# Kernel tuning notes

Hardware: AMD Instinct MI355X
Metric: run time of the kernel (lower is better)

The kernel has to match this reference:

```python
import jax, jax.numpy as jnp
import numpy as np

B, S, E, H = 4, 1024, 1024, 16
D = E // H  # head_dim = 64


def setup_inputs() -> dict:
    key = jax.random.key(0)
    ks = jax.random.split(key, 12)
    s = 1.0 / np.sqrt(E)
    return {
        "query": jax.random.normal(ks[0], (B, S, E), jnp.float32),
        "key_": jax.random.normal(ks[1], (B, S, E), jnp.float32),
        "value": jax.random.normal(ks[2], (B, S, E), jnp.float32),
        "mask": jnp.ones((B, S, S), dtype=bool),
        "Wq": jax.random.uniform(ks[3], (E, E), jnp.float32, -s, s),
        "bq": jax.random.uniform(ks[4], (E,), jnp.float32, -s, s),
        "Wk": jax.random.uniform(ks[5], (E, E), jnp.float32, -s, s),
        "bk": jax.random.uniform(ks[6], (E,), jnp.float32, -s, s),
        "Wv": jax.random.uniform(ks[7], (E, E), jnp.float32, -s, s),
        "bv": jax.random.uniform(ks[8], (E,), jnp.float32, -s, s),
        "Wo": jax.random.uniform(ks[9], (E, E), jnp.float32, -s, s),
        "bo": jax.random.uniform(ks[10], (E,), jnp.float32, -s, s),
    }


def reference(query, key_, value, mask, Wq, bq, Wk, bk, Wv, bv, Wo, bo):
    # project and split heads: [B,S,E] -> [B,H,S,D]
    def heads(x, W, b):
        return (x @ W + b).reshape(B, -1, H, D).transpose(0, 2, 1, 3)

    q = heads(query, Wq, bq)
    k = heads(key_, Wk, bk)
    v = heads(value, Wv, bv)

    scores = jnp.einsum("bhqd,bhkd->bhqk", q, k) / jnp.sqrt(jnp.float32(D))
    # bool mask: positions where mask==0 are filled with -1e9
    scores = jnp.where(mask[:, None, :, :], scores, jnp.float32(-1e9))
    attn_weights = jax.nn.softmax(scores, axis=-1)  # [B,H,Sq,Sk]
    out = jnp.einsum("bhqk,bhkd->bhqd", attn_weights, v)
    out = out.transpose(0, 2, 1, 3).reshape(B, -1, E)  # [B,Sq,E]
    attn_output = out @ Wo + bo
    return attn_output, attn_weights
```

## Files before the change

### kernel.cpp

```cpp
#include <hip/hip_runtime.h>
#include <stdint.h>

typedef __bf16 bf16;
typedef bf16 bf16x2 __attribute__((ext_vector_type(2)));
typedef bf16 bf16x4 __attribute__((ext_vector_type(4)));
typedef bf16 bf16x8 __attribute__((ext_vector_type(8)));
typedef float f32x4 __attribute__((ext_vector_type(4)));
typedef float f32x16 __attribute__((ext_vector_type(16)));

static constexpr int Bc = 4, Sc = 1024, Ec = 1024, Hc = 16, Dc = 64, BSc = 4096;

__device__ __forceinline__ void gld_lds16(const void* g, void* s) {
  __builtin_amdgcn_global_load_lds((const __attribute__((address_space(1))) void*)g,
                                   (__attribute__((address_space(3))) void*)s, 16, 0, 0);
}

__global__ void detect_mask_kernel(const uint8_t* __restrict__ mask, int* flag) {
  if (threadIdx.x == 0 && blockIdx.x == 0) {
    bool everyGroupHasZero = true;
    bool anyNonzero = false;
    for (int j = 0; j < 16; ++j) {
      bool z = false;
      for (int bjj = 0; bjj < 4; ++bjj) {
        uint8_t byte = mask[4 * j + bjj];
        if (byte == 0) z = true;
        if (byte != 0) anyNonzero = true;
      }
      if (!z) everyGroupHasZero = false;
    }
    flag[0] = (everyGroupHasZero && anyNonzero) ? 4 : 1;
    flag[1] = 1;
  }
}

__global__ __launch_bounds__(256) void scan_mask_kernel(const uint8_t* __restrict__ mask,
                                                        int* __restrict__ mflag) {
  const int stride = mflag[0];
  bool ok = true;
  const uint4* p = (const uint4*)mask;
  if (stride == 1) {
    const int n = (Bc * Sc * Sc) / 16;
    for (int i = blockIdx.x * blockDim.x + threadIdx.x; i < n; i += gridDim.x * blockDim.x) {
      uint4 w = p[i];
      uint32_t z = 0;
      z |= (w.x - 0x01010101u) & ~w.x;
      z |= (w.y - 0x01010101u) & ~w.y;
      z |= (w.z - 0x01010101u) & ~w.z;
      z |= (w.w - 0x01010101u) & ~w.w;
      if (z & 0x80808080u) ok = false;
    }
  } else {
    const int n = (Bc * Sc * Sc) / 4;
    for (int i = blockIdx.x * blockDim.x + threadIdx.x; i < n; i += gridDim.x * blockDim.x) {
      uint4 w = p[i];
      if (w.x == 0u || w.y == 0u || w.z == 0u || w.w == 0u) ok = false;
    }
  }
  if (!ok) atomicAnd(&mflag[1], 0);
}

__global__ __launch_bounds__(256) void convert_x_kernel(
    const float* __restrict__ q, const float* __restrict__ k, const float* __restrict__ v,
    bf16* __restrict__ xb) {
  const int n4 = (BSc * Ec) / 4;
  for (int i = blockIdx.x * blockDim.x + threadIdx.x; i < 3 * n4; i += gridDim.x * blockDim.x) {
    int which = i / n4;
    int off = i - which * n4;
    const float4* src = (which == 0) ? (const float4*)q : (which == 1) ? (const float4*)k : (const float4*)v;
    float4 f = src[off];
    bf16x4 o;
    o[0] = (bf16)f.x; o[1] = (bf16)f.y; o[2] = (bf16)f.z; o[3] = (bf16)f.w;
    *(bf16x4*)(xb + (size_t)which * BSc * Ec + (size_t)off * 4) = o;
  }
}

__global__ __launch_bounds__(256) void convtrans_w_kernel(
    const float* __restrict__ Wq, const float* __restrict__ Wk,
    const float* __restrict__ Wv, const float* __restrict__ Wo,
    bf16* __restrict__ wT) {
  __shared__ float tile[64][65];
  const int k0 = blockIdx.x * 64, n0 = blockIdx.y * 64, z = blockIdx.z;
  const float* W = (z == 0) ? Wq : (z == 1) ? Wk : (z == 2) ? Wv : Wo;
  bf16* out = wT + (size_t)z * Ec * Ec;
  const int t = threadIdx.x;
#pragma unroll
  for (int p = 0; p < 16; p++) {
    int r = p * 4 + (t >> 6), c = t & 63;
    tile[r][c] = W[(size_t)(k0 + r) * Ec + n0 + c];
  }
  __syncthreads();
#pragma unroll
  for (int p = 0; p < 8; p++) {
    int n = p * 8 + (t >> 5), kk = (t & 31) * 2;
    bf16x2 v2;
    v2[0] = (bf16)tile[kk][n];
    v2[1] = (bf16)tile[kk + 1][n];
    *(bf16x2*)(out + (size_t)(n0 + n) * Ec + k0 + kk) = v2;
  }
}

template <int MODE>
__global__ __launch_bounds__(256) void gemm128_kernel(
    const bf16* __restrict__ A_, const bf16* __restrict__ W_,
    const float* __restrict__ bias0, const float* __restrict__ bias1, const float* __restrict__ bias2,
    bf16* __restrict__ outb_, float* __restrict__ outf) {
  constexpr int K = 1024, N = 1024;
  const int z = blockIdx.z;
  const bf16* A = A_ + (size_t)z * BSc * K;
  const bf16* Wt = W_ + (size_t)z * N * K;
  const float* bias = (z == 0) ? bias0 : (z == 1) ? bias1 : bias2;
  bf16* outb = outb_ + (size_t)z * Bc * Hc * Sc * Dc;
  const float oscale = (MODE == 1 && z == 0) ? 0.125f : 1.0f;
  const int n0 = blockIdx.x * 128, m0 = blockIdx.y * 128;

  __shared__ bf16 As[128 * 64];
  __shared__ bf16 Bs[128 * 64];
  const int t = threadIdx.x, wave = t >> 6, lane = t & 63;
  const int wr = wave >> 1, wc = wave & 1;

  f32x4 acc[4][4];
#pragma unroll
  for (int i = 0; i < 4; i++)
#pragma unroll
    for (int j = 0; j < 4; j++)
#pragma unroll
      for (int r = 0; r < 4; r++) acc[i][j][r] = 0.f;

  const int srow = (lane >> 3);
  const int scol = (lane & 7) * 8;

  for (int kt = 0; kt < K; kt += 64) {
#pragma unroll
    for (int i = 0; i < 4; i++) {
      const int chunk = i * 4 + wave;
      const int row = chunk * 8 + srow;
      gld_lds16(A + (size_t)(m0 + row) * K + kt + scol, &As[chunk * 512]);
      gld_lds16(Wt + (size_t)(n0 + row) * K + kt + scol, &Bs[chunk * 512]);
    }
    __syncthreads();
#pragma unroll
    for (int kk = 0; kk < 2; kk++) {
      bf16x8 af[4], bg[4];
#pragma unroll
      for (int i = 0; i < 4; i++) {
        af[i] = *(const bf16x8*)&As[(64 * wr + i * 16 + (lane & 15)) * 64 + kk * 32 + (lane >> 4) * 8];
        bg[i] = *(const bf16x8*)&Bs[(64 * wc + i * 16 + (lane & 15)) * 64 + kk * 32 + (lane >> 4) * 8];
      }
#pragma unroll
      for (int mi = 0; mi < 4; mi++)
#pragma unroll
        for (int ni = 0; ni < 4; ni++)
          acc[mi][ni] = __builtin_amdgcn_mfma_f32_16x16x32_bf16(af[mi], bg[ni], acc[mi][ni], 0, 0, 0);
    }
    __syncthreads();
  }

#pragma unroll
  for (int mi = 0; mi < 4; mi++) {
#pragma unroll
    for (int ni = 0; ni < 4; ni++) {
      const int col = n0 + 64 * wc + ni * 16 + (lane & 15);
      const float bvl = bias[col];
#pragma unroll
      for (int r = 0; r < 4; r++) {
        const int row = m0 + 64 * wr + mi * 16 + (lane >> 4) * 4 + r;
        const float v = (acc[mi][ni][r] + bvl) * oscale;
        if (MODE == 0) {
          outf[(size_t)row * N + col] = v;
        } else {
          const int bidx = row >> 10, s = row & 1023, hh = col >> 6, d = col & 63;
          const int dst = (z == 1) ? (d ^ ((s & 7) << 3)) : d;
          outb[(((size_t)bidx * Hc + hh) * Sc + s) * Dc + dst] = (bf16)v;
        }
      }
    }
  }
}

__global__ __launch_bounds__(256) void transpose_v_kernel(const bf16* __restrict__ Vb,
                                                          bf16* __restrict__ VTb) {
  __shared__ bf16 tile[64][66];
  const int s0 = blockIdx.x * 64, bh = blockIdx.y;
  const bf16* src = Vb + (size_t)bh * Sc * Dc;
  bf16* dst = VTb + (size_t)bh * Dc * Sc;
  const int t = threadIdx.x;
#pragma unroll
  for (int p = 0; p < 8; p++) {
    int s = p * 8 + (t >> 5), d = (t & 31) * 2;
    *(bf16x2*)&tile[s][d] = *(const bf16x2*)(src + (size_t)(s0 + s) * Dc + d);
  }
  __syncthreads();
#pragma unroll
  for (int p = 0; p < 8; p++) {
    int d = p * 8 + (t >> 5), s = (t & 31) * 2;
    bf16x2 v2;
    v2[0] = tile[s][d];
    v2[1] = tile[s + 1][d];
    const int sidx = (s0 + s) ^ ((d & 7) << 3);
    *(bf16x2*)(dst + (size_t)d * Sc + sidx) = v2;
  }
}

__device__ __forceinline__ f32x16 qk_lds(const char* sK, const bf16x8 qf[4],
                                         int koff, int l31, int hi) {
  const int row = koff + l31;
  const char* base = sK + row * 128;
  const int sw = (row & 7) << 4;
  f32x16 a;
#pragma unroll
  for (int r = 0; r < 16; r++) a[r] = 0.f;
#pragma unroll
  for (int ks = 0; ks < 4; ks++) {
    const bf16x8 kf = *(const bf16x8*)(base + ((ks * 32 + hi * 16) ^ sw));
    a = __builtin_amdgcn_mfma_f32_32x32x16_bf16(kf, qf[ks], a, 0, 0, 0);
  }
  return a;
}

__device__ __forceinline__ void mask_app(f32x16& a, int kt, const uint8_t* mrow1,
                                         const uint8_t* mrow4, int mstride, int hi) {
  if (mstride == 1) {
#pragma unroll
    for (int gg = 0; gg < 4; gg++) {
      const int kg = kt + gg * 8 + hi * 4;
      const uint32_t mw = *(const uint32_t*)(mrow1 + kg);
#pragma unroll
      for (int r = 0; r < 4; r++)
        if (((mw >> (8 * r)) & 0xffu) == 0u) a[gg * 4 + r] = -1e9f;
    }
  } else {
#pragma unroll
    for (int gg = 0; gg < 4; gg++) {
      const int kg = kt + gg * 8 + hi * 4;
      const uint4 m4 = *(const uint4*)(mrow4 + (size_t)4 * kg);
      const uint32_t w[4] = {m4.x, m4.y, m4.z, m4.w};
#pragma unroll
      for (int r = 0; r < 4; r++)
        if (w[r] == 0u) a[gg * 4 + r] = -1e9f;
    }
  }
}

__global__ __launch_bounds__(256, 2) void attn_kernel(
    const bf16* __restrict__ Qb, const bf16* __restrict__ Kb, const bf16* __restrict__ VTb,
    const uint8_t* __restrict__ mask, const int* __restrict__ mflag,
    float* __restrict__ wout_, bf16* __restrict__ ctx) {
  const int qg = blockIdx.x, h = blockIdx.y, b = blockIdx.z;
  const int bh = b * Hc + h;
  const int t = threadIdx.x, wave = t >> 6, lane = t & 63;
  const int l31 = lane & 31, hi = lane >> 5;
  const int q0 = qg * 128 + wave * 32;
  const int q = q0 + l31;

  __shared__ __attribute__((aligned(16))) char smem[75776];
  bf16* Ptb = (bf16*)(smem + 65536) + wave * 1280;

  const bf16* Qp = Qb + ((size_t)bh * Sc + q) * Dc;
  bf16x8 qf[4];
#pragma unroll
  for (int ks = 0; ks < 4; ks++) qf[ks] = *(const bf16x8*)(Qp + ks * 16 + hi * 8);

  const int allTrue = mflag[1];
  const int mstride = mflag[0];
  const uint8_t* mrow1 = mask + (size_t)(b * Sc + q) * Sc;
  const uint8_t* mrow4 = mask + (size_t)(b * Sc + q) * Sc * 4;

  const char* Kbb = (const char*)(Kb + (size_t)bh * Sc * Dc);
  const char* VTbb = (const char*)(VTb + (size_t)bh * Dc * Sc);

  float m = -3.0e38f, l = 0.f;
#pragma unroll
  for (int j = 0; j < 4; j++) {
    const int off = j * 4096 + wave * 1024;
    gld_lds16(Kbb + off + lane * 16, smem + off);
  }
  __syncthreads();
  for (int st8 = 0; st8 < 8; st8++) {
    const int cur = st8 & 1;
    if (st8 < 7) {
#pragma unroll
      for (int j = 0; j < 4; j++) {
        const int off = j * 4096 + wave * 1024;
        gld_lds16(Kbb + (st8 + 1) * 16384 + off + lane * 16,
                  smem + (cur ^ 1) * 16384 + off);
      }
    }
    const char* sK = smem + cur * 16384;
#pragma unroll
    for (int tl = 0; tl < 4; tl++) {
      f32x16 a = qk_lds(sK, qf, tl * 32, l31, hi);
      if (!allTrue) mask_app(a, st8 * 128 + tl * 32, mrow1, mrow4, mstride, hi);
      float tm = a[0];
#pragma unroll
      for (int r = 1; r < 16; r++) tm = fmaxf(tm, a[r]);
      const float mnew = fmaxf(m, tm);
      float s = 0.f;
#pragma unroll
      for (int r = 0; r < 16; r++) s += __expf(a[r] - mnew);
      l = l * __expf(m - mnew) + s;
      m = mnew;
    }
    __syncthreads();
  }
  {
    const float mo = __shfl_xor(m, 32), lo = __shfl_xor(l, 32);
    const float M = fmaxf(m, mo);
    l = l * __expf(m - M) + lo * __expf(mo - M);
    m = M;
  }
  const float invl = 1.f / l;

  float* wbase = wout_ + ((size_t)bh * Sc + q0) * Sc;
  f32x16 oacc[2];
#pragma unroll
  for (int nj = 0; nj < 2; nj++)
#pragma unroll
    for (int r = 0; r < 16; r++) oacc[nj][r] = 0.f;

#pragma unroll
  for (int j = 0; j < 4; j++) {
    const int off = j * 4096 + wave * 1024;
    gld_lds16(Kbb + off + lane * 16, smem + off);
    const int goff = off + lane * 16;
    const int d = goff >> 8, ko = goff & 255;
    gld_lds16(VTbb + (size_t)d * 2048 + ko, smem + 32768 + off);
  }
  __syncthreads();
  for (int st8 = 0; st8 < 8; st8++) {
    const int cur = st8 & 1;
    if (st8 < 7) {
#pragma unroll
      for (int j = 0; j < 4; j++) {
        const int off = j * 4096 + wave * 1024;
        gld_lds16(Kbb + (st8 + 1) * 16384 + off + lane * 16,
                  smem + (cur ^ 1) * 16384 + off);
        const int goff = off + lane * 16;
        const int d = goff >> 8, ko = goff & 255;
        gld_lds16(VTbb + (size_t)d * 2048 + (st8 + 1) * 256 + ko,
                  smem + 32768 + (cur ^ 1) * 16384 + off);
      }
    }
    const char* sK = smem + cur * 16384;
    const char* sV = smem + 32768 + cur * 16384;
#pragma unroll
    for (int tl = 0; tl < 4; tl++) {
      f32x16 a = qk_lds(sK, qf, tl * 32, l31, hi);
      if (!allTrue) mask_app(a, st8 * 128 + tl * 32, mrow1, mrow4, mstride, hi);
#pragma unroll
      for (int gg = 0; gg < 4; gg++) {
        bf16x4 p4;
#pragma unroll
        for (int r = 0; r < 4; r++) p4[r] = (bf16)(__expf(a[gg * 4 + r] - m) * invl);
        *(bf16x4*)&Ptb[l31 * 40 + gg * 8 + hi * 4] = p4;
      }
#pragma unroll
      for (int i = 0; i < 4; i++) {
        const int q2 = 8 * i + (lane >> 3), kk = (lane & 7) * 4;
        const bf16x4 pv4 = *(const bf16x4*)&Ptb[q2 * 40 + kk];
        f32x4 v4;
#pragma unroll
        for (int r = 0; r < 4; r++) v4[r] = (float)pv4[r];
        __builtin_nontemporal_store(v4,
            (f32x4*)(wbase + (size_t)q2 * Sc + st8 * 128 + tl * 32 + kk));
      }
#pragma unroll
      for (int st = 0; st < 2; st++) {
        const bf16x8 pa = *(const bf16x8*)&Ptb[l31 * 40 + st * 16 + hi * 8];
#pragma unroll
        for (int nj = 0; nj < 2; nj++) {
          const int d = nj * 32 + l31;
          const int off = ((tl * 32 + st * 16 + hi * 8) * 2) ^ ((d & 7) << 4);
          const bf16x8 bv = *(const bf16x8*)(sV + d * 256 + off);
          oacc[nj] = __builtin_amdgcn_mfma_f32_32x32x16_bf16(pa, bv, oacc[nj], 0, 0, 0);
        }
      }
    }
    __syncthreads();
  }

#pragma unroll
  for (int nj = 0; nj < 2; nj++) {
#pragma unroll
    for (int rg = 0; rg < 16; rg++) {
      const int qq = (rg & 3) + 8 * (rg >> 2) + 4 * hi;
      Ptb[qq * 40 + l31] = (bf16)oacc[nj][rg];
    }
    const int rr = lane >> 1, c0 = (lane & 1) * 16;
    const bf16x8 o0 = *(const bf16x8*)&Ptb[rr * 40 + c0];
    const bf16x8 o1 = *(const bf16x8*)&Ptb[rr * 40 + c0 + 8];
    bf16* cbase = ctx + ((size_t)(b * Sc + q0 + rr)) * Ec + h * Dc + nj * 32 + c0;
    *(bf16x8*)cbase = o0;
    *(bf16x8*)(cbase + 8) = o1;
  }
}

extern "C" void kernel_launch(void* const* d_in, const int* in_sizes, int n_in,
                              void* d_out, int out_size, void* d_ws, size_t ws_size,
                              hipStream_t stream) {
  const float* q = (const float*)d_in[0];
  const float* k = (const float*)d_in[1];
  const float* v = (const float*)d_in[2];
  const uint8_t* mask = (const uint8_t*)d_in[3];
  const float* Wq = (const float*)d_in[4];
  const float* bq = (const float*)d_in[5];
  const float* Wk = (const float*)d_in[6];
  const float* bk = (const float*)d_in[7];
  const float* Wv = (const float*)d_in[8];
  const float* bv = (const float*)d_in[9];
  const float* Wo = (const float*)d_in[10];
  const float* bo = (const float*)d_in[11];

  bf16* wsb = (bf16*)d_ws;
  bf16* xb = wsb;
  bf16* ctx = wsb;
  bf16* VTb = wsb + (size_t)4 * 1024 * 1024;
  bf16* wT = wsb + (size_t)12 * 1024 * 1024;
  bf16* Qb = wsb + (size_t)16 * 1024 * 1024;
  bf16* Kb = wsb + (size_t)20 * 1024 * 1024;
  bf16* Vb = wsb + (size_t)24 * 1024 * 1024;
  int* mflag = (int*)((char*)d_ws + (size_t)56 * 1024 * 1024);

  float* outf = (float*)d_out;
  float* attnw = outf + (size_t)4 * 1024 * 1024;

  detect_mask_kernel<<<1, 64, 0, stream>>>(mask, mflag);
  scan_mask_kernel<<<1024, 256, 0, stream>>>(mask, mflag);
  convert_x_kernel<<<2048, 256, 0, stream>>>(q, k, v, xb);
  convtrans_w_kernel<<<dim3(16, 16, 4), 256, 0, stream>>>(Wq, Wk, Wv, Wo, wT);
  gemm128_kernel<1><<<dim3(8, 32, 3), 256, 0, stream>>>(xb, wT, bq, bk, bv, Qb, nullptr);
  transpose_v_kernel<<<dim3(16, 64), 256, 0, stream>>>(Vb, VTb);
  attn_kernel<<<dim3(8, 16, 4), 256, 0, stream>>>(Qb, Kb, VTb, mask, mflag, attnw, ctx);
  gemm128_kernel<0><<<dim3(8, 32, 1), 256, 0, stream>>>(ctx, wT + (size_t)3 * 1024 * 1024,
                                                        bo, bo, bo, nullptr, outf);
}
```

Before: 192.4 us.

## Merge prep kernels into one launch and halve attention K/V tiles for occupancy

Folds the mask scan, the activation conversion and the weight transpose-convert into one prep kernel, cutting two launches and letting these independent jobs overlap. The scan blocks now recompute the mask stride themselves instead of reading it from the flag buffer. The attention kernel streams K/V in 64-key tiles rather than 128, roughly halving LDS use so three blocks fit per CU instead of two. The cost is twice as many barrier/prefetch iterations in attention and more register pressure under the tighter launch bound.

```diff
diff --git a/kernel.cpp b/kernel.cpp
--- a/kernel.cpp
+++ b/kernel.cpp
@@ -33,69 +33,79 @@
   }
 }
 
-__global__ __launch_bounds__(256) void scan_mask_kernel(const uint8_t* __restrict__ mask,
-                                                        int* __restrict__ mflag) {
-  const int stride = mflag[0];
-  bool ok = true;
-  const uint4* p = (const uint4*)mask;
-  if (stride == 1) {
-    const int n = (Bc * Sc * Sc) / 16;
-    for (int i = blockIdx.x * blockDim.x + threadIdx.x; i < n; i += gridDim.x * blockDim.x) {
-      uint4 w = p[i];
-      uint32_t z = 0;
-      z |= (w.x - 0x01010101u) & ~w.x;
-      z |= (w.y - 0x01010101u) & ~w.y;
-      z |= (w.z - 0x01010101u) & ~w.z;
-      z |= (w.w - 0x01010101u) & ~w.w;
-      if (z & 0x80808080u) ok = false;
-    }
+__global__ __launch_bounds__(256) void prep_kernel(
+    const float* __restrict__ q, const float* __restrict__ k, const float* __restrict__ v,
+    bf16* __restrict__ xb, const uint8_t* __restrict__ mask, int* __restrict__ mflag,
+    const float* __restrict__ Wq, const float* __restrict__ Wk,
+    const float* __restrict__ Wv, const float* __restrict__ Wo, bf16* __restrict__ wT) {
+  __shared__ float tile[64][65];
+  const int bid = blockIdx.x, t = threadIdx.x;
+
+  if (bid < 2048) {
+    const int n4 = (BSc * Ec) / 4;
+    for (int i = bid * 256 + t; i < 3 * n4; i += 2048 * 256) {
+      int which = i / n4;
+      int off = i - which * n4;
+      const float4* src = (which == 0) ? (const float4*)q : (which == 1) ? (const float4*)k : (const float4*)v;
+      float4 f = src[off];
+      bf16x4 o;
+      o[0] = (bf16)f.x; o[1] = (bf16)f.y; o[2] = (bf16)f.z; o[3] = (bf16)f.w;
+      *(bf16x4*)(xb + (size_t)which * BSc * Ec + (size_t)off * 4) = o;
+    }
+  } else if (bid < 3072) {
+    bool everyGroupHasZero = true, anyNonzero = false;
+    for (int j = 0; j < 16; ++j) {
+      bool z = false;
+      for (int bjj = 0; bjj < 4; ++bjj) {
+        uint8_t byte = mask[4 * j + bjj];
+        if (byte == 0) z = true;
+        if (byte != 0) anyNonzero = true;
+      }
+      if (!z) everyGroupHasZero = false;
+    }
+    const int stride = (everyGroupHasZero && anyNonzero) ? 4 : 1;
+    bool ok = true;
+    const uint4* p = (const uint4*)mask;
+    const int sb = bid - 2048;
+    if (stride == 1) {
+      const int n = (Bc * Sc * Sc) / 16;
+      for (int i = sb * 256 + t; i < n; i += 1024 * 256) {
+        uint4 w = p[i];
+        uint32_t z = 0;
+        z |= (w.x - 0x01010101u) & ~w.x;
+        z |= (w.y - 0x01010101u) & ~w.y;
+        z |= (w.z - 0x01010101u) & ~w.z;
+        z |= (w.w - 0x01010101u) & ~w.w;
+        if (z & 0x80808080u) ok = false;
+      }
+    } else {
+      const int n = (Bc * Sc * Sc) / 4;
+      for (int i = sb * 256 + t; i < n; i += 1024 * 256) {
+        uint4 w = p[i];
+        if (w.x == 0u || w.y == 0u || w.z == 0u || w.w == 0u) ok = false;
+      }
+    }
+    if (!ok) atomicAnd(&mflag[1], 0);
   } else {
-    const int n = (Bc * Sc * Sc) / 4;
-    for (int i = blockIdx.x * blockDim.x + threadIdx.x; i < n; i += gridDim.x * blockDim.x) {
-      uint4 w = p[i];
-      if (w.x == 0u || w.y == 0u || w.z == 0u || w.w == 0u) ok = false;
-    }
-  }
-  if (!ok) atomicAnd(&mflag[1], 0);
-}
-
-__global__ __launch_bounds__(256) void convert_x_kernel(
-    const float* __restrict__ q, const float* __restrict__ k, const float* __restrict__ v,
-    bf16* __restrict__ xb) {
-  const int n4 = (BSc * Ec) / 4;
-  for (int i = blockIdx.x * blockDim.x + threadIdx.x; i < 3 * n4; i += gridDim.x * blockDim.x) {
-    int which = i / n4;
-    int off = i - which * n4;
-    const float4* src = (which == 0) ? (const float4*)q : (which == 1) ? (const float4*)k : (const float4*)v;
-    float4 f = src[off];
-    bf16x4 o;
-    o[0] = (bf16)f.x; o[1] = (bf16)f.y; o[2] = (bf16)f.z; o[3] = (bf16)f.w;
-    *(bf16x4*)(xb + (size_t)which * BSc * Ec + (size_t)off * 4) = o;
-  }
-}
-
-__global__ __launch_bounds__(256) void convtrans_w_kernel(
-    const float* __restrict__ Wq, const float* __restrict__ Wk,
-    const float* __restrict__ Wv, const float* __restrict__ Wo,
-    bf16* __restrict__ wT) {
-  __shared__ float tile[64][65];
-  const int k0 = blockIdx.x * 64, n0 = blockIdx.y * 64, z = blockIdx.z;
-  const float* W = (z == 0) ? Wq : (z == 1) ? Wk : (z == 2) ? Wv : Wo;
-  bf16* out = wT + (size_t)z * Ec * Ec;
-  const int t = threadIdx.x;
-#pragma unroll
-  for (int p = 0; p < 16; p++) {
-    int r = p * 4 + (t >> 6), c = t & 63;
-    tile[r][c] = W[(size_t)(k0 + r) * Ec + n0 + c];
-  }
-  __syncthreads();
-#pragma unroll
-  for (int p = 0; p < 8; p++) {
-    int n = p * 8 + (t >> 5), kk = (t & 31) * 2;
-    bf16x2 v2;
-    v2[0] = (bf16)tile[kk][n];
-    v2[1] = (bf16)tile[kk + 1][n];
-    *(bf16x2*)(out + (size_t)(n0 + n) * Ec + k0 + kk) = v2;
+    const int i = bid - 3072;
+    const int z = i >> 8, rem = i & 255;
+    const int k0 = (rem & 15) * 64, n0 = (rem >> 4) * 64;
+    const float* W = (z == 0) ? Wq : (z == 1) ? Wk : (z == 2) ? Wv : Wo;
+    bf16* out = wT + (size_t)z * Ec * Ec;
+#pragma unroll
+    for (int p2 = 0; p2 < 16; p2++) {
+      int r = p2 * 4 + (t >> 6), c = t & 63;
+      tile[r][c] = W[(size_t)(k0 + r) * Ec + n0 + c];
+    }
+    __syncthreads();
+#pragma unroll
+    for (int p2 = 0; p2 < 8; p2++) {
+      int n = p2 * 8 + (t >> 5), kk = (t & 31) * 2;
+      bf16x2 v2;
+      v2[0] = (bf16)tile[kk][n];
+      v2[1] = (bf16)tile[kk + 1][n];
+      *(bf16x2*)(out + (size_t)(n0 + n) * Ec + k0 + kk) = v2;
+    }
   }
 }
 
@@ -241,7 +251,7 @@
   }
 }
 
-__global__ __launch_bounds__(256, 2) void attn_kernel(
+__global__ __launch_bounds__(256, 3) void attn_kernel(
     const bf16* __restrict__ Qb, const bf16* __restrict__ Kb, const bf16* __restrict__ VTb,
     const uint8_t* __restrict__ mask, const int* __restrict__ mflag,
     float* __restrict__ wout_, bf16* __restrict__ ctx) {
@@ -252,8 +262,8 @@
   const int q0 = qg * 128 + wave * 32;
   const int q = q0 + l31;
 
-  __shared__ __attribute__((aligned(16))) char smem[75776];
-  bf16* Ptb = (bf16*)(smem + 65536) + wave * 1280;
+  __shared__ __attribute__((aligned(16))) char smem[43008];
+  bf16* Ptb = (bf16*)(smem + 32768) + wave * 1280;
 
   const bf16* Qp = Qb + ((size_t)bh * Sc + q) * Dc;
   bf16x8 qf[4];
@@ -270,26 +280,25 @@
 
   float m = -3.0e38f, l = 0.f;
 #pragma unroll
-  for (int j = 0; j < 4; j++) {
+  for (int j = 0; j < 2; j++) {
     const int off = j * 4096 + wave * 1024;
     gld_lds16(Kbb + off + lane * 16, smem + off);
   }
   __syncthreads();
-  for (int st8 = 0; st8 < 8; st8++) {
-    const int cur = st8 & 1;
-    if (st8 < 7) {
-#pragma unroll
-      for (int j = 0; j < 4; j++) {
+  for (int st = 0; st < 16; st++) {
+    const int cur = st & 1;
+    if (st < 15) {
+#pragma unroll
+      for (int j = 0; j < 2; j++) {
         const int off = j * 4096 + wave * 1024;
-        gld_lds16(Kbb + (st8 + 1) * 16384 + off + lane * 16,
-                  smem + (cur ^ 1) * 16384 + off);
-      }
-    }
-    const char* sK = smem + cur * 16384;
-#pragma unroll
-    for (int tl = 0; tl < 4; tl++) {
+        gld_lds16(Kbb + (st + 1) * 8192 + off + lane * 16, smem + (cur ^ 1) * 8192 + off);
+      }
+    }
+    const char* sK = smem + cur * 8192;
+#pragma unroll
+    for (int tl = 0; tl < 2; tl++) {
       f32x16 a = qk_lds(sK, qf, tl * 32, l31, hi);
-      if (!allTrue) mask_app(a, st8 * 128 + tl * 32, mrow1, mrow4, mstride, hi);
+      if (!allTrue) mask_app(a, st * 64 + tl * 32, mrow1, mrow4, mstride, hi);
       float tm = a[0];
 #pragma unroll
       for (int r = 1; r < 16; r++) tm = fmaxf(tm, a[r]);
@@ -318,34 +327,33 @@
     for (int r = 0; r < 16; r++) oacc[nj][r] = 0.f;
 
 #pragma unroll
-  for (int j = 0; j < 4; j++) {
+  for (int j = 0; j < 2; j++) {
     const int off = j * 4096 + wave * 1024;
     gld_lds16(Kbb + off + lane * 16, smem + off);
     const int goff = off + lane * 16;
-    const int d = goff >> 8, ko = goff & 255;
-    gld_lds16(VTbb + (size_t)d * 2048 + ko, smem + 32768 + off);
+    const int d = goff >> 7, ko = goff & 127;
+    gld_lds16(VTbb + (size_t)d * 2048 + ko, smem + 16384 + off);
   }
   __syncthreads();
-  for (int st8 = 0; st8 < 8; st8++) {
-    const int cur = st8 & 1;
-    if (st8 < 7) {
-#pragma unroll
-      for (int j = 0; j < 4; j++) {
+  for (int st = 0; st < 16; st++) {
+    const int cur = st & 1;
+    if (st < 15) {
+#pragma unroll
+      for (int j = 0; j < 2; j++) {
         const int off = j * 4096 + wave * 1024;
-        gld_lds16(Kbb + (st8 + 1) * 16384 + off + lane * 16,
-                  smem + (cur ^ 1) * 16384 + off);
+        gld_lds16(Kbb + (st + 1) * 8192 + off + lane * 16, smem + (cur ^ 1) * 8192 + off);
         const int goff = off + lane * 16;
-        const int d = goff >> 8, ko = goff & 255;
-        gld_lds16(VTbb + (size_t)d * 2048 + (st8 + 1) * 256 + ko,
-                  smem + 32768 + (cur ^ 1) * 16384 + off);
-      }
-    }
-    const char* sK = smem + cur * 16384;
-    const char* sV = smem + 32768 + cur * 16384;
-#pragma unroll
-    for (int tl = 0; tl < 4; tl++) {
+        const int d = goff >> 7, ko = goff & 127;
+        gld_lds16(VTbb + (size_t)d * 2048 + (st + 1) * 128 + ko,
+                  smem + 16384 + (cur ^ 1) * 8192 + off);
+      }
+    }
+    const char* sK = smem + cur * 8192;
+    const char* sV = smem + 16384 + cur * 8192;
+#pragma unroll
+    for (int tl = 0; tl < 2; tl++) {
       f32x16 a = qk_lds(sK, qf, tl * 32, l31, hi);
-      if (!allTrue) mask_app(a, st8 * 128 + tl * 32, mrow1, mrow4, mstride, hi);
+      if (!allTrue) mask_app(a, st * 64 + tl * 32, mrow1, mrow4, mstride, hi);
 #pragma unroll
       for (int gg = 0; gg < 4; gg++) {
         bf16x4 p4;
@@ -361,16 +369,16 @@
 #pragma unroll
         for (int r = 0; r < 4; r++) v4[r] = (float)pv4[r];
         __builtin_nontemporal_store(v4,
-            (f32x4*)(wbase + (size_t)q2 * Sc + st8 * 128 + tl * 32 + kk));
-      }
-#pragma unroll
-      for (int st = 0; st < 2; st++) {
-        const bf16x8 pa = *(const bf16x8*)&Ptb[l31 * 40 + st * 16 + hi * 8];
+            (f32x4*)(wbase + (size_t)q2 * Sc + st * 64 + tl * 32 + kk));
+      }
+#pragma unroll
+      for (int stq = 0; stq < 2; stq++) {
+        const bf16x8 pa = *(const bf16x8*)&Ptb[l31 * 40 + stq * 16 + hi * 8];
 #pragma unroll
         for (int nj = 0; nj < 2; nj++) {
           const int d = nj * 32 + l31;
-          const int off = ((tl * 32 + st * 16 + hi * 8) * 2) ^ ((d & 7) << 4);
-          const bf16x8 bv = *(const bf16x8*)(sV + d * 256 + off);
+          const int off = ((tl * 32 + stq * 16 + hi * 8) * 2) ^ ((d & 7) << 4);
+          const bf16x8 bv = *(const bf16x8*)(sV + d * 128 + off);
           oacc[nj] = __builtin_amdgcn_mfma_f32_32x32x16_bf16(pa, bv, oacc[nj], 0, 0, 0);
         }
       }
@@ -424,9 +432,7 @@
   float* attnw = outf + (size_t)4 * 1024 * 1024;
 
   detect_mask_kernel<<<1, 64, 0, stream>>>(mask, mflag);
-  scan_mask_kernel<<<1024, 256, 0, stream>>>(mask, mflag);
-  convert_x_kernel<<<2048, 256, 0, stream>>>(q, k, v, xb);
-  convtrans_w_kernel<<<dim3(16, 16, 4), 256, 0, stream>>>(Wq, Wk, Wv, Wo, wT);
+  prep_kernel<<<4096, 256, 0, stream>>>(q, k, v, xb, mask, mflag, Wq, Wk, Wv, Wo, wT);
   gemm128_kernel<1><<<dim3(8, 32, 3), 256, 0, stream>>>(xb, wT, bq, bk, bv, Qb, nullptr);
   transpose_v_kernel<<<dim3(16, 64), 256, 0, stream>>>(Vb, VTb);
   attn_kernel<<<dim3(8, 16, 4), 256, 0, stream>>>(Qb, Kb, VTb, mask, mflag, attnw, ctx);
```

Result: faster. 188.1 us (-2.2%).
